# Kernel optimization log

Hardware: AMD Instinct MI355X
Metric: run time of the kernel (lower is better)

## Reference

```python
import jax, jax.numpy as jnp
import numpy as np

B, L, D, K = 8, 1024, 1024, 128
VOCAB, N_ATOM_FEAT, N_TIMESTEPS = 160, 512, 1000
NEG = jnp.finfo(jnp.float32).min
SCALING = K ** (-0.5)


def setup_inputs() -> dict:
    key = jax.random.key(0)
    ks = jax.random.split(key, 14)
    inp = {}
    # forward args
    inp["token_id"] = jax.random.randint(ks[0], (B, L), 0, VOCAB)  # 0 => padding
    inp["node_attr"] = jax.random.randint(ks[1], (B, L, 9), 0, N_ATOM_FEAT)
    inp["is_molecule"] = jax.random.randint(ks[2], (B,), 0, 2).astype(bool)
    inp["pos"] = jax.random.normal(ks[3], (B, L, 3), jnp.float32) * 10.0
    inp["time_step"] = jax.random.randint(ks[4], (B, L), 0, N_TIMESTEPS)
    # learned parameters
    inp["embed_table"] = jax.random.normal(ks[5], (VOCAB, D), jnp.float32) * 0.02
    inp["atom_feat_table"] = jax.random.normal(ks[6], (N_ATOM_FEAT, D), jnp.float32) * 0.02
    inp["time_table"] = jax.random.normal(ks[7], (N_TIMESTEPS, D), jnp.float32) * 0.02
    inp["time_w1"] = jax.random.normal(ks[8], (D, D), jnp.float32) * (D ** -0.5)
    inp["time_b1"] = jnp.zeros((D,), jnp.float32)
    inp["time_w2"] = jax.random.normal(ks[9], (D, D), jnp.float32) * (D ** -0.5)
    inp["time_b2"] = jnp.zeros((D,), jnp.float32)
    inp["pos_emb_w"] = jax.random.normal(ks[10], (1, K), jnp.float32)          # Linear(1 -> K), no bias
    inp["pos_feature_w"] = jax.random.normal(ks[11], (K, D), jnp.float32) * (K ** -0.5)  # Linear(K -> D), no bias
    return inp


def _pos_emb(pos, padding_mask, pos_emb_w, pos_feature_w):
    # pos: [B,L,3], padding_mask: [B,L] bool
    delta = pos[:, :, None, :] - pos[:, None, :, :]          # [B,L,L,3]
    dist = 1.0 / (jnp.linalg.norm(delta, axis=-1) + 1.0)     # [B,L,L]
    # masked_fill on key side (expand_mask) and query side (padding_mask)
    mask = padding_mask[:, None, :] | padding_mask[:, :, None]
    dist = jnp.where(mask, NEG, dist)
    # value projection: Linear(1->K) on per-atom radial norm, zeroed at padding
    pe = jnp.linalg.norm(pos, axis=-1, keepdims=True) @ pos_emb_w  # [B,L,K]
    pe = jnp.where(padding_mask[:, :, None], 0.0, pe)
    attn = jax.nn.softmax(dist * SCALING, axis=-1)            # [B,L,L]
    pfe = jnp.einsum("bqk,bkc->bqc", attn, pe)                 # [B,L,K]
    pfe = pfe @ pos_feature_w                                  # [B,L,D]
    return jnp.where(padding_mask[:, :, None], 0.0, pfe)


def reference(token_id, node_attr, is_molecule, pos, time_step,
              embed_table, atom_feat_table, time_table,
              time_w1, time_b1, time_w2, time_b2,
              pos_emb_w, pos_feature_w):
    padding_mask = token_id == 0                               # [B,L]
    x = embed_table[token_id]                                  # [B,L,D]
    # 2D atom features: embed cols 1: and sum over feature axis
    atom_emb = atom_feat_table[node_attr[:, :, 1:]].sum(axis=-2)  # [B,L,D]
    atom_emb = jnp.where(is_molecule[:, None, None], atom_emb, 0.0)
    x = x + atom_emb
    # time step encoder: learnable embedding + Linear-SiLU-Linear MLP
    t = time_table[time_step]                                   # [B,L,D]
    time_embed = jax.nn.silu(t @ time_w1 + time_b1) @ time_w2 + time_b2
    x = x + time_embed
    # pairwise 3D positional embedding (softmax attention over 1/(r+1))
    x = x + _pos_emb(pos, padding_mask, pos_emb_w, pos_feature_w)
    return x, padding_mask
```

## Files before the change

### kernel.cpp

```cpp
#include <hip/hip_runtime.h>
#include <hip/hip_bf16.h>
#include <math.h>

#define BB 8
#define LL 1024
#define DD 1024
#define KK 128
#define NTS 1000
#define VOCAB 160
#define NATOM 512
#define SCALE 0.08838834764831845f

typedef __attribute__((ext_vector_type(8))) short short8;
typedef __attribute__((ext_vector_type(4))) float f32x4;

__device__ __forceinline__ unsigned short f2bf(float x) {
    __hip_bfloat16 h = __float2bfloat16(x);
    return *reinterpret_cast<unsigned short*>(&h);
}
__device__ __forceinline__ float bf2f(unsigned short u) {
    return __uint_as_float(((unsigned int)u) << 16);
}

__global__ __launch_bounds__(256) void prep_kernel(
    const float* __restrict__ w1,
    const float* __restrict__ w2,
    const float* __restrict__ embed_f,
    const float* __restrict__ atom_f,
    const float* __restrict__ pos_emb_w,
    const float* __restrict__ pos_feature_w,
    const void*  __restrict__ is_mol_raw,
    unsigned short* __restrict__ W1t,
    unsigned short* __restrict__ W2t,
    unsigned short* __restrict__ embed_bf,
    unsigned short* __restrict__ atom_bf,
    float* __restrict__ v,
    int*   __restrict__ is_mol_out)
{
    __shared__ float tile[32][33];
    const int blk = blockIdx.x;

    if (blk < 2048) {
        const int which = blk >> 10;
        const int idx = blk & 1023;
        const float* in = which ? w2 : w1;
        unsigned short* out = which ? W2t : W1t;
        const int bx = (idx & 31) * 32, by = (idx >> 5) * 32;
        const int tx = threadIdx.x & 31, ty = threadIdx.x >> 5;
        #pragma unroll
        for (int r = 0; r < 32; r += 8)
            tile[ty + r][tx] = in[(size_t)(by + ty + r) * DD + bx + tx];
        __syncthreads();
        #pragma unroll
        for (int r = 0; r < 32; r += 8)
            out[(size_t)(bx + ty + r) * DD + by + tx] = f2bf(tile[tx][ty + r]);
    } else if (blk < 2208) {
        const int e = ((blk - 2048) * 256 + threadIdx.x) * 4;
        float4 vv = *(const float4*)&embed_f[e];
        ushort4 o = { f2bf(vv.x), f2bf(vv.y), f2bf(vv.z), f2bf(vv.w) };
        *(ushort4*)&embed_bf[e] = o;
    } else if (blk < 2720) {
        const int e = ((blk - 2208) * 256 + threadIdx.x) * 4;
        float4 vv = *(const float4*)&atom_f[e];
        ushort4 o = { f2bf(vv.x), f2bf(vv.y), f2bf(vv.z), f2bf(vv.w) };
        *(ushort4*)&atom_bf[e] = o;
    } else if (blk < 2724) {
        int d = (blk - 2720) * 256 + threadIdx.x;
        float acc = 0.0f;
        #pragma unroll 4
        for (int c = 0; c < KK; ++c)
            acc += pos_emb_w[c] * pos_feature_w[c * DD + d];
        v[d] = acc;
    } else {
        if (threadIdx.x == 0) {
            const int* ip = (const int*)is_mol_raw;
            const unsigned char* cp = (const unsigned char*)is_mol_raw;
            bool all_bin = true;
            for (int i = 0; i < BB; ++i) {
                int x = ip[i];
                if (x != 0 && x != 1) all_bin = false;
            }
            for (int i = 0; i < BB; ++i)
                is_mol_out[i] = all_bin ? (ip[i] != 0) : (cp[i] != 0);
        }
    }
}

template <int MODE>
__global__ __launch_bounds__(256) void mfma_gemm32(
    const void* __restrict__ Ap,
    const unsigned short* __restrict__ Bt,
    const float* __restrict__ bias,
    unsigned short* __restrict__ Cout)
{
    __shared__ __align__(16) unsigned short As[32][72];
    __shared__ __align__(16) unsigned short Bs[32][72];

    const int tid  = threadIdx.x;
    const int lane = tid & 63;
    const int wave = tid >> 6;
    const int wm = wave >> 1, wn = wave & 1;
    const int quad = lane >> 4, l16 = lane & 15;
    const int mBase = blockIdx.y * 32, nBase = blockIdx.x * 32;

    f32x4 acc = {0.f, 0.f, 0.f, 0.f};

    const int r = tid >> 3, ko = (tid & 7) * 8;
    const int rowB = nBase + r;
    int rowA = mBase + r;
    if (MODE == 0 && rowA >= NTS) rowA = NTS - 1;

    for (int k0 = 0; k0 < DD; k0 += 64) {
        if (MODE == 0) {
            const float* A = (const float*)Ap;
            float4 a0 = *(const float4*)&A[(size_t)rowA * DD + k0 + ko];
            float4 a1 = *(const float4*)&A[(size_t)rowA * DD + k0 + ko + 4];
            short8 s8;
            s8[0] = f2bf(a0.x); s8[1] = f2bf(a0.y); s8[2] = f2bf(a0.z); s8[3] = f2bf(a0.w);
            s8[4] = f2bf(a1.x); s8[5] = f2bf(a1.y); s8[6] = f2bf(a1.z); s8[7] = f2bf(a1.w);
            *(short8*)&As[r][ko] = s8;
        } else {
            const unsigned short* A = (const unsigned short*)Ap;
            *(float4*)&As[r][ko] = *(const float4*)&A[(size_t)rowA * DD + k0 + ko];
        }
        *(float4*)&Bs[r][ko] = *(const float4*)&Bt[(size_t)rowB * DD + k0 + ko];
        __syncthreads();

        #pragma unroll
        for (int kk = 0; kk < 64; kk += 32) {
            short8 af = *(const short8*)&As[wm * 16 + l16][kk + quad * 8];
            short8 bf = *(const short8*)&Bs[wn * 16 + l16][kk + quad * 8];
            acc = __builtin_amdgcn_mfma_f32_16x16x32_bf16(af, bf, acc, 0, 0, 0);
        }
        __syncthreads();
    }

    const int col = nBase + wn * 16 + l16;
    const float bv = bias[col];
    #pragma unroll
    for (int r4 = 0; r4 < 4; ++r4) {
        const int row = mBase + wm * 16 + quad * 4 + r4;
        float val = acc[r4] + bv;
        if (MODE == 0) val = val / (1.0f + __expf(-val));
        Cout[(size_t)row * DD + col] = f2bf(val);
    }
}

__global__ __launch_bounds__(256) void fused_all(
    const int*   __restrict__ token_id,
    const int*   __restrict__ node_attr,
    const float* __restrict__ pos,
    const int*   __restrict__ time_step,
    const unsigned short* __restrict__ embed_bf,
    const unsigned short* __restrict__ atom_bf,
    const unsigned short* __restrict__ Ebf,
    const float* __restrict__ v,
    const int*   __restrict__ is_mol,
    float* __restrict__ out)
{
    __shared__ float4 keys[LL];
    __shared__ float  sS[8];

    const int blk   = blockIdx.x;
    const int batch = blk >> 7;
    const int q0    = (blk & 127) << 3;
    const int tid   = threadIdx.x;
    const int lane  = tid & 63, wave = tid >> 6;

    #pragma unroll
    for (int i = 0; i < 4; ++i) {
        const int k = tid + i * 256;
        const int t = batch * LL + k;
        const float x = pos[t * 3 + 0];
        const float y = pos[t * 3 + 1];
        const float z = pos[t * 3 + 2];
        const int tok = token_id[t];
        const float n = sqrtf(x * x + y * y + z * z);
        keys[k] = make_float4(x, y, z, tok == 0 ? -1.0f : n);
    }
    __syncthreads();

    #pragma unroll
    for (int qi = 0; qi < 2; ++qi) {
        const int ql = wave * 2 + qi;
        const float4 qk = keys[q0 + ql];
        float lsum = 0.0f, lws = 0.0f;
        #pragma unroll 4
        for (int i = 0; i < 16; ++i) {
            const float4 kd = keys[lane + i * 64];
            const float dx = qk.x - kd.x, dy = qk.y - kd.y, dz = qk.z - kd.z;
            const float dn = sqrtf(dx * dx + dy * dy + dz * dz);
            const float e = __expf(SCALE / (dn + 1.0f));
            const bool valid = kd.w >= 0.0f;
            const float ev = valid ? e : 0.0f;
            lsum += ev;
            lws  += ev * (valid ? kd.w : 0.0f);
        }
        #pragma unroll
        for (int off = 32; off > 0; off >>= 1) {
            lsum += __shfl_xor(lsum, off);
            lws  += __shfl_xor(lws,  off);
        }
        if (lane == 0)
            sS[ql] = (qk.w < 0.0f) ? 0.0f : (lws / lsum);
    }
    __syncthreads();

    const int im   = is_mol[batch];
    const int half = tid >> 7;
    const int tl   = tid & 127;
    const int j    = tl * 8;
    const float4 v0 = *(const float4*)&v[j];
    const float4 v1 = *(const float4*)&v[j + 4];

    #pragma unroll
    for (int qp = 0; qp < 4; ++qp) {
        const int ql  = qp * 2 + half;
        const int t   = batch * LL + q0 + ql;
        const int tok = token_id[t];
        const int ts  = time_step[t];
        const float s = sS[ql];

        float o[8];
        short8 eb = *(const short8*)&embed_bf[(size_t)tok * DD + j];
        #pragma unroll
        for (int d = 0; d < 8; ++d) o[d] = bf2f((unsigned short)eb[d]);

        if (im) {
            #pragma unroll
            for (int f = 1; f < 9; ++f) {
                const int a = node_attr[t * 9 + f];
                short8 ab = *(const short8*)&atom_bf[(size_t)a * DD + j];
                #pragma unroll
                for (int d = 0; d < 8; ++d) o[d] += bf2f((unsigned short)ab[d]);
            }
        }
        short8 er = *(const short8*)&Ebf[(size_t)ts * DD + j];
        #pragma unroll
        for (int d = 0; d < 8; ++d) o[d] += bf2f((unsigned short)er[d]);

        o[0] += s * v0.x; o[1] += s * v0.y; o[2] += s * v0.z; o[3] += s * v0.w;
        o[4] += s * v1.x; o[5] += s * v1.y; o[6] += s * v1.z; o[7] += s * v1.w;

        float4 w0 = {o[0], o[1], o[2], o[3]};
        float4 w1 = {o[4], o[5], o[6], o[7]};
        *(float4*)&out[(size_t)t * DD + j]     = w0;
        *(float4*)&out[(size_t)t * DD + j + 4] = w1;
    }

    if (tid < 8) {
        const int t = batch * LL + q0 + tid;
        out[(size_t)BB * LL * DD + t] = (keys[q0 + tid].w < 0.0f) ? 1.0f : 0.0f;
    }
}

extern "C" void kernel_launch(void* const* d_in, const int* in_sizes, int n_in,
                              void* d_out, int out_size, void* d_ws, size_t ws_size,
                              hipStream_t stream)
{
    const int*   token_id      = (const int*)  d_in[0];
    const int*   node_attr     = (const int*)  d_in[1];
    const void*  is_mol_raw    = (const void*) d_in[2];
    const float* pos           = (const float*)d_in[3];
    const int*   time_step     = (const int*)  d_in[4];
    const float* embed_table   = (const float*)d_in[5];
    const float* atom_feat     = (const float*)d_in[6];
    const float* time_table    = (const float*)d_in[7];
    const float* w1            = (const float*)d_in[8];
    const float* b1            = (const float*)d_in[9];
    const float* w2            = (const float*)d_in[10];
    const float* b2            = (const float*)d_in[11];
    const float* pos_emb_w     = (const float*)d_in[12];
    const float* pos_feature_w = (const float*)d_in[13];

    float* out = (float*)d_out;
    char*  ws  = (char*)d_ws;

    unsigned short* W1t      = (unsigned short*)(ws);
    unsigned short* Ebf      = (unsigned short*)(ws);
    unsigned short* H        = (unsigned short*)(ws + (2u << 20));
    unsigned short* W2t      = (unsigned short*)(ws + (4u << 20));
    unsigned short* embed_bf = (unsigned short*)(ws + (6u << 20));
    unsigned short* atom_bf  = (unsigned short*)(ws + (6u << 20) + (512u << 10));
    float*          V        = (float*)(ws + (7u << 20) + (512u << 10));
    int*            is_mol_r = (int*)(V + 1024);

    prep_kernel<<<2725, 256, 0, stream>>>(w1, w2, embed_table, atom_feat,
                                          pos_emb_w, pos_feature_w, is_mol_raw,
                                          W1t, W2t, embed_bf, atom_bf,
                                          V, is_mol_r);

    dim3 g(32, 32);
    mfma_gemm32<0><<<g, 256, 0, stream>>>((const void*)time_table, W1t, b1, H);
    mfma_gemm32<1><<<g, 256, 0, stream>>>((const void*)H,          W2t, b2, Ebf);

    fused_all<<<1024, 256, 0, stream>>>(token_id, node_attr, pos, time_step,
                                        embed_bf, atom_bf, Ebf, V,
                                        is_mol_r, out);
}
```

Before: 151.7 us.

## Keep full B tile resident in LDS and stream A directly from global

The two time-MLP GEMMs now load a 32x1024 slice of the transposed weight into shared memory once per block. They then loop over the full K dimension, reading A fragments straight from global memory into registers, with no per-step syncthreads. Each block computes two 32-row M tiles, so the grid is halved. This removes the per-K-step barriers and the A staging through LDS, but it uses a large LDS footprint (about 66KB), which limits occupancy. It also relies on uncoalesced, strided per-lane global reads of A, and the two waves sharing an M row read the same A data redundantly.

```diff
diff --git a/kernel.cpp b/kernel.cpp
--- a/kernel.cpp
+++ b/kernel.cpp
@@ -87,62 +87,67 @@
 }
 
 template <int MODE>
-__global__ __launch_bounds__(256) void mfma_gemm32(
+__global__ __launch_bounds__(256) void gemm_bres(
     const void* __restrict__ Ap,
     const unsigned short* __restrict__ Bt,
     const float* __restrict__ bias,
     unsigned short* __restrict__ Cout)
 {
-    __shared__ __align__(16) unsigned short As[32][72];
-    __shared__ __align__(16) unsigned short Bs[32][72];
+    __shared__ __align__(16) unsigned short Bs[32][1032];
 
     const int tid  = threadIdx.x;
     const int lane = tid & 63;
     const int wave = tid >> 6;
     const int wm = wave >> 1, wn = wave & 1;
     const int quad = lane >> 4, l16 = lane & 15;
-    const int mBase = blockIdx.y * 32, nBase = blockIdx.x * 32;
-
-    f32x4 acc = {0.f, 0.f, 0.f, 0.f};
-
-    const int r = tid >> 3, ko = (tid & 7) * 8;
-    const int rowB = nBase + r;
-    int rowA = mBase + r;
-    if (MODE == 0 && rowA >= NTS) rowA = NTS - 1;
-
-    for (int k0 = 0; k0 < DD; k0 += 64) {
-        if (MODE == 0) {
-            const float* A = (const float*)Ap;
-            float4 a0 = *(const float4*)&A[(size_t)rowA * DD + k0 + ko];
-            float4 a1 = *(const float4*)&A[(size_t)rowA * DD + k0 + ko + 4];
-            short8 s8;
-            s8[0] = f2bf(a0.x); s8[1] = f2bf(a0.y); s8[2] = f2bf(a0.z); s8[3] = f2bf(a0.w);
-            s8[4] = f2bf(a1.x); s8[5] = f2bf(a1.y); s8[6] = f2bf(a1.z); s8[7] = f2bf(a1.w);
-            *(short8*)&As[r][ko] = s8;
-        } else {
-            const unsigned short* A = (const unsigned short*)Ap;
-            *(float4*)&As[r][ko] = *(const float4*)&A[(size_t)rowA * DD + k0 + ko];
-        }
-        *(float4*)&Bs[r][ko] = *(const float4*)&Bt[(size_t)rowB * DD + k0 + ko];
-        __syncthreads();
-
-        #pragma unroll
-        for (int kk = 0; kk < 64; kk += 32) {
-            short8 af = *(const short8*)&As[wm * 16 + l16][kk + quad * 8];
-            short8 bf = *(const short8*)&Bs[wn * 16 + l16][kk + quad * 8];
-            acc = __builtin_amdgcn_mfma_f32_16x16x32_bf16(af, bf, acc, 0, 0, 0);
-        }
-        __syncthreads();
-    }
+    const int nBase = blockIdx.x * 32;
+
+    {
+        const int r = tid >> 3;
+        const int kb = (tid & 7) * 128;
+        #pragma unroll
+        for (int c = 0; c < 16; ++c)
+            *(float4*)&Bs[r][kb + c * 8] =
+                *(const float4*)&Bt[(size_t)(nBase + r) * DD + kb + c * 8];
+    }
+    __syncthreads();
 
     const int col = nBase + wn * 16 + l16;
     const float bv = bias[col];
+    const int kq = quad * 8;
+
     #pragma unroll
-    for (int r4 = 0; r4 < 4; ++r4) {
-        const int row = mBase + wm * 16 + quad * 4 + r4;
-        float val = acc[r4] + bv;
-        if (MODE == 0) val = val / (1.0f + __expf(-val));
-        Cout[(size_t)row * DD + col] = f2bf(val);
+    for (int mt = 0; mt < 2; ++mt) {
+        const int mBase = blockIdx.y * 64 + mt * 32;
+        int rowA = mBase + wm * 16 + l16;
+        if (MODE == 0 && rowA >= NTS) rowA = NTS - 1;
+
+        f32x4 acc = {0.f, 0.f, 0.f, 0.f};
+
+        #pragma unroll 4
+        for (int kk = 0; kk < DD; kk += 32) {
+            short8 af;
+            if (MODE == 0) {
+                const float* A = (const float*)Ap;
+                float4 a0 = *(const float4*)&A[(size_t)rowA * DD + kk + kq];
+                float4 a1 = *(const float4*)&A[(size_t)rowA * DD + kk + kq + 4];
+                af[0]=f2bf(a0.x); af[1]=f2bf(a0.y); af[2]=f2bf(a0.z); af[3]=f2bf(a0.w);
+                af[4]=f2bf(a1.x); af[5]=f2bf(a1.y); af[6]=f2bf(a1.z); af[7]=f2bf(a1.w);
+            } else {
+                const unsigned short* A = (const unsigned short*)Ap;
+                af = *(const short8*)&A[(size_t)rowA * DD + kk + kq];
+            }
+            short8 bf = *(const short8*)&Bs[wn * 16 + l16][kk + kq];
+            acc = __builtin_amdgcn_mfma_f32_16x16x32_bf16(af, bf, acc, 0, 0, 0);
+        }
+
+        #pragma unroll
+        for (int r4 = 0; r4 < 4; ++r4) {
+            const int row = mBase + wm * 16 + quad * 4 + r4;
+            float val = acc[r4] + bv;
+            if (MODE == 0) val = val / (1.0f + __expf(-val));
+            Cout[(size_t)row * DD + col] = f2bf(val);
+        }
     }
 }
 
@@ -290,9 +295,9 @@
                                           W1t, W2t, embed_bf, atom_bf,
                                           V, is_mol_r);
 
-    dim3 g(32, 32);
-    mfma_gemm32<0><<<g, 256, 0, stream>>>((const void*)time_table, W1t, b1, H);
-    mfma_gemm32<1><<<g, 256, 0, stream>>>((const void*)H,          W2t, b2, Ebf);
+    dim3 g(32, 16);
+    gemm_bres<0><<<g, 256, 0, stream>>>((const void*)time_table, W1t, b1, H);
+    gemm_bres<1><<<g, 256, 0, stream>>>((const void*)H,          W2t, b2, Ebf);
 
     fused_all<<<1024, 256, 0, stream>>>(token_id, node_attr, pos, time_step,
                                         embed_bf, atom_bf, Ebf, V,
```

Measured after the change: 181.7 us. 1.2x slower.
